# Performance work log

Measured on AMD Instinct MI355X. Metric: run time of the kernel, lower is better.

Reference implementation:

```python
import jax, jax.numpy as jnp
import numpy as np

B, S, DIM = 2, 2048, 2048
H, DH = 16, 128
FF = 4 * DIM
EPS = 1e-5


def layer_norm(x, w, b, eps=EPS):
    m = jnp.mean(x, axis=-1, keepdims=True)
    v = jnp.mean(jnp.square(x - m), axis=-1, keepdims=True)
    return (x - m) * jax.lax.rsqrt(v + eps) * w + b


def apply_rotary(x, cos, sin):
    # x: [B, H, S, DH]; cos/sin: [S, DH//2]; complex multiply on (even, odd) pairs
    x2 = x.reshape(*x.shape[:-1], DH // 2, 2)
    x0, x1 = x2[..., 0], x2[..., 1]
    c = cos[None, None, :, :]
    s = sin[None, None, :, :]
    r0 = x0 * c - x1 * s
    r1 = x0 * s + x1 * c
    return jnp.stack([r0, r1], axis=-1).reshape(x.shape)


def setup_inputs() -> dict:
    key = jax.random.key(0)
    ks = jax.random.split(key, 16)
    sc = 0.02
    pos = jnp.arange(S, dtype=jnp.float32)[:, None]
    inv_freq = 1.0 / (10000.0 ** (jnp.arange(0, DH // 2, dtype=jnp.float32) / (DH // 2)))
    ang = pos * inv_freq[None, :]
    return {
        "hidden_states": jax.random.normal(ks[0], (B, S, DIM), jnp.float32),
        "freqs_cos": jnp.cos(ang),
        "freqs_sin": jnp.sin(ang),
        "wq": jax.random.normal(ks[1], (DIM, H * DH), jnp.float32) * sc,
        "wk": jax.random.normal(ks[2], (DIM, H * DH), jnp.float32) * sc,
        "wv": jax.random.normal(ks[3], (DIM, H * DH), jnp.float32) * sc,
        "nq_w": jnp.ones((DH,), jnp.float32),
        "nq_b": jnp.zeros((DH,), jnp.float32),
        "nk_w": jnp.ones((DH,), jnp.float32),
        "nk_b": jnp.zeros((DH,), jnp.float32),
        "wo": jax.random.normal(ks[4], (H * DH, DIM), jnp.float32) * sc,
        "bo": jnp.zeros((DIM,), jnp.float32),
        "ln1_w": jnp.ones((DIM,), jnp.float32),
        "ln1_b": jnp.zeros((DIM,), jnp.float32),
        "ln3_w": jnp.ones((DIM,), jnp.float32),
        "ln3_b": jnp.zeros((DIM,), jnp.float32),
        "w1": jax.random.normal(ks[5], (DIM, FF), jnp.float32) * sc,
        "b1": jnp.zeros((FF,), jnp.float32),
        "w2": jax.random.normal(ks[6], (FF, DIM), jnp.float32) * sc,
        "b2": jnp.zeros((DIM,), jnp.float32),
    }


def reference(hidden_states, freqs_cos, freqs_sin, wq, wk, wv, nq_w, nq_b, nk_w, nk_b,
              wo, bo, ln1_w, ln1_b, ln3_w, ln3_b, w1, b1, w2, b2):
    x = hidden_states
    # --- self-attention branch ---
    n = layer_norm(x, ln1_w, ln1_b)                       # [B,S,DIM]
    q = (n @ wq).reshape(B, S, H, DH)
    k = (n @ wk).reshape(B, S, H, DH)
    v = (n @ wv).reshape(B, S, H, DH)
    # per-head QK LayerNorm (norm over dim_head)
    q = layer_norm(q, nq_w, nq_b)
    k = layer_norm(k, nk_w, nk_b)
    q = q.transpose(0, 2, 1, 3)                            # [B,H,S,DH]
    k = k.transpose(0, 2, 1, 3)
    v = v.transpose(0, 2, 1, 3)
    q = apply_rotary(q, freqs_cos, freqs_sin)
    k = apply_rotary(k, freqs_cos, freqs_sin)
    scale = DH ** -0.5
    scores = jnp.einsum("bhqd,bhkd->bhqk", q, k) * scale   # [B,H,S,S]
    probs = jax.nn.softmax(scores, axis=-1)
    attn = jnp.einsum("bhqk,bhkd->bhqd", probs, v)         # [B,H,S,DH]
    attn = attn.transpose(0, 2, 1, 3).reshape(B, S, H * DH)
    x = x + (attn @ wo + bo)
    # --- feed-forward branch ---
    n = layer_norm(x, ln3_w, ln3_b)
    h = jax.nn.gelu(n @ w1 + b1, approximate=False)
    x = x + (h @ w2 + b2)
    return x
```

## Files before the change

kernel.cpp:

```cpp
#include <hip/hip_runtime.h>
#include <hip/hip_bf16.h>
#include <stdint.h>

typedef __hip_bfloat16 bf16;
typedef float v4f __attribute__((ext_vector_type(4)));
typedef short v8s __attribute__((ext_vector_type(8)));

#define DEV __device__ __forceinline__

DEV float b2f(bf16 x) { return __bfloat162float(x); }
DEV bf16 f2b(float x) { return __float2bfloat16(x); }

DEV void load4(const float* p, float* f) {
  float4 t = *(const float4*)p;
  f[0] = t.x; f[1] = t.y; f[2] = t.z; f[3] = t.w;
}
DEV void load4(const bf16* p, float* f) {
  union { uint2 u; bf16 h[4]; } t;
  t.u = *(const uint2*)p;
#pragma unroll
  for (int i = 0; i < 4; i++) f[i] = b2f(t.h[i]);
}
DEV void load8(const float* p, float* f) {
  float4 a = ((const float4*)p)[0], b = ((const float4*)p)[1];
  f[0] = a.x; f[1] = a.y; f[2] = a.z; f[3] = a.w;
  f[4] = b.x; f[5] = b.y; f[6] = b.z; f[7] = b.w;
}
DEV void load8(const bf16* p, float* f) {
  union { uint4 u; bf16 h[8]; } t;
  t.u = *(const uint4*)p;
#pragma unroll
  for (int i = 0; i < 8; i++) f[i] = b2f(t.h[i]);
}
DEV void store4(bf16* p, const float* f) {
  union { uint2 u; bf16 h[4]; } t;
#pragma unroll
  for (int i = 0; i < 4; i++) t.h[i] = f2b(f[i]);
  *(uint2*)p = t.u;
}
DEV void store4(float* p, const float* f) {
  *(float4*)p = make_float4(f[0], f[1], f[2], f[3]);
}

DEV void gld_lds16(const bf16* g, bf16* l) {
  auto gp = reinterpret_cast<const __attribute__((address_space(1))) uint32_t*>(
      reinterpret_cast<uintptr_t>(g));
  auto lp = reinterpret_cast<__attribute__((address_space(3))) uint32_t*>(
      reinterpret_cast<uintptr_t>(l));
  __builtin_amdgcn_global_load_lds(gp, lp, 16, 0, 0);
}

template <typename XT>
__global__ __launch_bounds__(256)
void ln2048_kernel(const XT* __restrict__ x, const float* __restrict__ w,
                   const float* __restrict__ b, bf16* __restrict__ y) {
  const int N = 2048;
  int row = blockIdx.x, tid = threadIdx.x;
  const XT* xr = x + (size_t)row * N;
  bf16* yr = y + (size_t)row * N;
  float f[8], s = 0.f, ss = 0.f;
  load8(xr + tid * 8, f);
#pragma unroll
  for (int i = 0; i < 8; i++) { s += f[i]; ss += f[i] * f[i]; }
#pragma unroll
  for (int off = 32; off >= 1; off >>= 1) {
    s  += __shfl_xor(s, off, 64);
    ss += __shfl_xor(ss, off, 64);
  }
  __shared__ float red0[4], red1[4];
  int wv = tid >> 6;
  if ((tid & 63) == 0) { red0[wv] = s; red1[wv] = ss; }
  __syncthreads();
  s  = red0[0] + red0[1] + red0[2] + red0[3];
  ss = red1[0] + red1[1] + red1[2] + red1[3];
  float mean = s * (1.f / N);
  float var  = ss * (1.f / N) - mean * mean;
  float inv  = rsqrtf(var + 1e-5f);
  float wf[8], bf_[8];
  load8(w + tid * 8, wf);
  load8(b + tid * 8, bf_);
  union { uint4 u; bf16 h[8]; } vo;
#pragma unroll
  for (int i = 0; i < 8; i++)
    vo.h[i] = f2b((f[i] - mean) * inv * wf[i] + bf_[i]);
  ((uint4*)yr)[tid] = vo.u;
}

__global__ __launch_bounds__(256)
void headln_rope_kernel(bf16* __restrict__ q, const float* __restrict__ w,
                        const float* __restrict__ b, const float* __restrict__ fcos,
                        const float* __restrict__ fsin) {
  int tid = threadIdx.x;
  int wv = tid >> 6, ln = tid & 63;
  int idx = blockIdx.x * 4 + wv;
  int row = idx >> 4, h = idx & 15;
  int srow = row & 2047;
  bf16* p = q + (size_t)row * 2048 + h * 128 + ln * 2;
  union { unsigned int u; bf16 h2[2]; } v;
  v.u = *(const unsigned int*)p;
  float x0 = b2f(v.h2[0]), x1 = b2f(v.h2[1]);
  float s = x0 + x1, ss = x0 * x0 + x1 * x1;
#pragma unroll
  for (int off = 32; off >= 1; off >>= 1) {
    s  += __shfl_xor(s, off, 64);
    ss += __shfl_xor(ss, off, 64);
  }
  float mean = s * (1.f / 128.f);
  float var  = ss * (1.f / 128.f) - mean * mean;
  float inv  = rsqrtf(var + 1e-5f);
  float w0 = w[ln * 2], w1 = w[ln * 2 + 1];
  float b0 = b[ln * 2], b1 = b[ln * 2 + 1];
  x0 = (x0 - mean) * inv * w0 + b0;
  x1 = (x1 - mean) * inv * w1 + b1;
  float c  = fcos[srow * 64 + ln];
  float sn = fsin[srow * 64 + ln];
  v.h2[0] = f2b(x0 * c - x1 * sn);
  v.h2[1] = f2b(x0 * sn + x1 * c);
  *(unsigned int*)p = v.u;
}

__global__ __launch_bounds__(256)
void convT_kernel(const float* __restrict__ src, bf16* __restrict__ dst,
                  int K, int N) {
  __shared__ float T[64][65];
  int n0 = blockIdx.x * 64, k0 = blockIdx.y * 64;
  int t = threadIdx.x;
  int tr = t >> 4, tc4 = (t & 15) * 4;
#pragma unroll
  for (int it = 0; it < 4; it++) {
    float4 v = *(const float4*)&src[(size_t)(k0 + tr + 16 * it) * N + n0 + tc4];
    T[tr + 16 * it][tc4 + 0] = v.x;
    T[tr + 16 * it][tc4 + 1] = v.y;
    T[tr + 16 * it][tc4 + 2] = v.z;
    T[tr + 16 * it][tc4 + 3] = v.w;
  }
  __syncthreads();
#pragma unroll
  for (int it = 0; it < 4; it++) {
    int n = tr + 16 * it;
    union { uint2 u; bf16 h[4]; } o;
#pragma unroll
    for (int c = 0; c < 4; c++) o.h[c] = f2b(T[tc4 + c][n]);
    *(uint2*)&dst[(size_t)(n0 + n) * K + k0 + tc4] = o.u;
  }
}

template <int EPI, typename RT, typename OT>
__global__ __launch_bounds__(256, 2)
void mfma_gemm_kernel(const bf16* __restrict__ A, const bf16* __restrict__ BT,
                      OT* __restrict__ C, const float* __restrict__ bias,
                      const RT* __restrict__ res, int M, int N, int K) {
  __shared__ __align__(16) bf16 As[128 * 32];
  __shared__ __align__(16) bf16 Bs[128 * 32];
  int tid = threadIdx.x;
  int lane = tid & 63, wave = tid >> 6;
  int wr = wave >> 1, wc = wave & 1;
  int m0 = blockIdx.y * 128, n0 = blockIdx.x * 128;

  int ls_row = lane >> 2;
  int ls_k   = (lane & 3) * 8;
  int t0 = 2 * wave, t1 = 2 * wave + 1;
  const bf16* gA0 = A  + (size_t)(m0 + 16 * t0 + ls_row) * K + ls_k;
  const bf16* gA1 = A  + (size_t)(m0 + 16 * t1 + ls_row) * K + ls_k;
  const bf16* gB0 = BT + (size_t)(n0 + 16 * t0 + ls_row) * K + ls_k;
  const bf16* gB1 = BT + (size_t)(n0 + 16 * t1 + ls_row) * K + ls_k;
  bf16* lA0 = As + t0 * 512;
  bf16* lA1 = As + t1 * 512;
  bf16* lB0 = Bs + t0 * 512;
  bf16* lB1 = Bs + t1 * 512;

  int fr = lane & 15, fk = (lane >> 4) * 8;
  const bf16* pA = As + (wr * 64 + fr) * 32 + fk;
  const bf16* pB = Bs + (wc * 64 + fr) * 32 + fk;

  v4f acc[4][4];
#pragma unroll
  for (int i = 0; i < 4; i++)
#pragma unroll
    for (int j = 0; j < 4; j++) acc[i][j] = (v4f){0.f, 0.f, 0.f, 0.f};

  for (int k0 = 0; k0 < K; k0 += 32) {
    __syncthreads();
    gld_lds16(gA0, lA0); gld_lds16(gA1, lA1);
    gld_lds16(gB0, lB0); gld_lds16(gB1, lB1);
    gA0 += 32; gA1 += 32; gB0 += 32; gB1 += 32;
    __syncthreads();
    v8s af[4], bfr[4];
#pragma unroll
    for (int i = 0; i < 4; i++) af[i]  = *(const v8s*)(pA + i * 16 * 32);
#pragma unroll
    for (int j = 0; j < 4; j++) bfr[j] = *(const v8s*)(pB + j * 16 * 32);
#pragma unroll
    for (int i = 0; i < 4; i++)
#pragma unroll
      for (int j = 0; j < 4; j++)
        acc[i][j] = __builtin_amdgcn_mfma_f32_16x16x32_bf16(af[i], bfr[j],
                                                            acc[i][j], 0, 0, 0);
  }

  int rq = (lane >> 4) * 4;
#pragma unroll
  for (int j = 0; j < 4; j++) {
    int n = n0 + wc * 64 + j * 16 + (lane & 15);
    float bb = (EPI >= 1) ? bias[n] : 0.f;
#pragma unroll
    for (int i = 0; i < 4; i++) {
#pragma unroll
      for (int r = 0; r < 4; r++) {
        int m = m0 + wr * 64 + i * 16 + rq + r;
        float val = acc[i][j][r] + bb;
        if (EPI == 2)
          val = 0.5f * val * (1.f + erff(val * 0.70710678118654752f));
        if (EPI == 1) {
          if constexpr (__is_same(RT, float)) val += res[(size_t)m * N + n];
          else                                val += b2f(res[(size_t)m * N + n]);
        }
        if constexpr (__is_same(OT, float)) C[(size_t)m * N + n] = val;
        else                                C[(size_t)m * N + n] = f2b(val);
      }
    }
  }
}

template <int EPI, typename RT, typename OT>
__global__ __launch_bounds__(256)
void gemm_kernel(const bf16* __restrict__ A, const float* __restrict__ Bm,
                 OT* __restrict__ C, const float* __restrict__ bias,
                 const RT* __restrict__ res, int M, int N, int K) {
  const int BK = 32;
  __shared__ __align__(16) float As[BK][68];
  __shared__ __align__(16) float Bs[BK][68];
  int tid = threadIdx.x;
  int bm = blockIdx.y, bn = blockIdx.x;
  int tx = tid & 15, ty = tid >> 4;
  int am = tid >> 2, ak8 = (tid & 3) * 8;
  int bkr = tid >> 3, bn8 = (tid & 7) * 8;
  const bf16* Aptr = A + (size_t)(bm * 64 + am) * K + ak8;
  const float* Bptr = Bm + (size_t)bkr * N + bn * 64 + bn8;
  float acc[4][4] = {};
  for (int k0 = 0; k0 < K; k0 += BK) {
    float av[8], bv[8];
    load8(Aptr, av);
    load8(Bptr, bv);
    __syncthreads();
#pragma unroll
    for (int j = 0; j < 8; j++) As[ak8 + j][am] = av[j];
#pragma unroll
    for (int j = 0; j < 8; j++) Bs[bkr][bn8 + j] = bv[j];
    __syncthreads();
    Aptr += BK;
    Bptr += (size_t)BK * N;
#pragma unroll 8
    for (int kk = 0; kk < BK; kk++) {
      float a0[4], b0[4];
      *(float4*)a0 = *(const float4*)&As[kk][ty * 4];
      *(float4*)b0 = *(const float4*)&Bs[kk][tx * 4];
#pragma unroll
      for (int i = 0; i < 4; i++)
#pragma unroll
        for (int j = 0; j < 4; j++)
          acc[i][j] += a0[i] * b0[j];
    }
  }
  int m0 = bm * 64 + ty * 4, n0 = bn * 64 + tx * 4;
#pragma unroll
  for (int i = 0; i < 4; i++) {
    float r4[4];
#pragma unroll
    for (int j = 0; j < 4; j++) r4[j] = acc[i][j];
    if (EPI >= 1) {
      float bb[4];
      load4(bias + n0, bb);
#pragma unroll
      for (int j = 0; j < 4; j++) r4[j] += bb[j];
    }
    if (EPI == 2) {
#pragma unroll
      for (int j = 0; j < 4; j++)
        r4[j] = 0.5f * r4[j] * (1.f + erff(r4[j] * 0.70710678118654752f));
    }
    if (EPI == 1) {
      float rr[4];
      load4(res + (size_t)(m0 + i) * N + n0, rr);
#pragma unroll
      for (int j = 0; j < 4; j++) r4[j] += rr[j];
    }
    store4(&C[(size_t)(m0 + i) * N + n0], r4);
  }
}

__global__ __launch_bounds__(256, 2)
void attn_kernel(const bf16* __restrict__ q, const bf16* __restrict__ k,
                 const bf16* __restrict__ v, bf16* __restrict__ o) {
  const int S = 2048, HD = 2048;
  __shared__ __align__(16) char smem[49664];
  char* KsB = smem;
  char* VtB = smem + 16384;
  char* QPB = smem + 32768;
  float* Lp = (float*)(smem + 49152);

  int id = blockIdx.x;
  int swzb = (id & 7) * 128 + (id >> 3);
  int bh = swzb >> 5, qb = swzb & 31;
  int q0 = qb * 64;
  size_t base = (size_t)(bh >> 4) * S * HD + (size_t)(bh & 15) * 128;

  int tid = threadIdx.x;
  int lane = tid & 63, wave = tid >> 6;
  int wr = wave >> 1, wc = wave & 1;
  int fr = lane & 15, fg = lane >> 4;

  if (tid < 128) Lp[tid] = 0.f;

#pragma unroll
  for (int t = 0; t < 4; t++) {
    int ti = wave * 4 + t;
    int r = ti * 4 + fg;
    int cb = (fr * 16) ^ ((r & 7) << 4);
    gld_lds16(q + base + (size_t)(q0 + r) * HD + (cb >> 1),
              (bf16*)QPB + ti * 512);
  }
  __syncthreads();
  v8s qfrag[2][4];
#pragma unroll
  for (int i = 0; i < 2; i++)
#pragma unroll
    for (int kk = 0; kk < 4; kk++) {
      int row = wr * 32 + i * 16 + fr;
      int off = row * 256 + ((kk * 64 + fg * 16) ^ ((row & 7) << 4));
      qfrag[i][kk] = *(const v8s*)(QPB + off);
    }

  v4f oacc[2][4];
#pragma unroll
  for (int i = 0; i < 2; i++)
#pragma unroll
    for (int j = 0; j < 4; j++) oacc[i][j] = (v4f){0.f, 0.f, 0.f, 0.f};

  const float scale = 0.08838834764831845f;
  int vr0 = (tid & 15) * 4, vd0 = (tid >> 4) * 8;

  for (int kt = 0; kt < S; kt += 64) {
    __syncthreads();
#pragma unroll
    for (int t = 0; t < 4; t++) {
      int ti = wave * 4 + t;
      int r = ti * 4 + fg;
      int cb = (fr * 16) ^ ((r & 7) << 4);
      gld_lds16(k + base + (size_t)(kt + r) * HD + (cb >> 1),
                (bf16*)KsB + ti * 512);
    }
    union { uint4 u; bf16 h[8]; } vrow[4];
#pragma unroll
    for (int j = 0; j < 4; j++)
      vrow[j].u = *(const uint4*)&v[base + (size_t)(kt + vr0 + j) * HD + vd0];
#pragma unroll
    for (int c = 0; c < 8; c++) {
      int d = vd0 + c;
      union { uint2 u; bf16 h[4]; } pk;
#pragma unroll
      for (int j = 0; j < 4; j++) pk.h[j] = vrow[j].h[c];
      *(uint2*)(VtB + d * 128 + ((vr0 * 2) ^ ((d & 7) << 4))) = pk.u;
    }
    __syncthreads();

    v4f sacc[2][2];
#pragma unroll
    for (int i = 0; i < 2; i++)
#pragma unroll
      for (int j = 0; j < 2; j++) sacc[i][j] = (v4f){0.f, 0.f, 0.f, 0.f};
#pragma unroll
    for (int kk = 0; kk < 4; kk++) {
      v8s kf[2];
#pragma unroll
      for (int j = 0; j < 2; j++) {
        int row = wc * 32 + j * 16 + fr;
        int off = row * 256 + ((kk * 64 + fg * 16) ^ ((row & 7) << 4));
        kf[j] = *(const v8s*)(KsB + off);
      }
#pragma unroll
      for (int i = 0; i < 2; i++)
#pragma unroll
        for (int j = 0; j < 2; j++)
          sacc[i][j] = __builtin_amdgcn_mfma_f32_16x16x32_bf16(
              qfrag[i][kk], kf[j], sacc[i][j], 0, 0, 0);
    }

#pragma unroll
    for (int i = 0; i < 2; i++)
#pragma unroll
      for (int r = 0; r < 4; r++) {
        int qrow = wr * 32 + i * 16 + fg * 4 + r;
        float e0 = __expf(sacc[i][0][r] * scale);
        float e1 = __expf(sacc[i][1][r] * scale);
        int sw = (qrow & 7) << 4;
        int c0 = wc * 64 + fr * 2;
        *(bf16*)(QPB + qrow * 128 + (c0 ^ sw))        = f2b(e0);
        *(bf16*)(QPB + qrow * 128 + ((c0 + 32) ^ sw)) = f2b(e1);
        float s = e0 + e1;
        s += __shfl_xor(s, 1, 64);
        s += __shfl_xor(s, 2, 64);
        s += __shfl_xor(s, 4, 64);
        s += __shfl_xor(s, 8, 64);
        if (fr == 0) Lp[wc * 64 + qrow] += s;
      }
    __syncthreads();

#pragma unroll
    for (int kk2 = 0; kk2 < 2; kk2++) {
      v8s pf[2], vf[4];
#pragma unroll
      for (int i = 0; i < 2; i++) {
        int row = wr * 32 + i * 16 + fr;
        int off = row * 128 + ((kk2 * 64 + fg * 16) ^ ((row & 7) << 4));
        pf[i] = *(const v8s*)(QPB + off);
      }
#pragma unroll
      for (int j = 0; j < 4; j++) {
        int row = wc * 64 + j * 16 + fr;
        int off = row * 128 + ((kk2 * 64 + fg * 16) ^ ((row & 7) << 4));
        vf[j] = *(const v8s*)(VtB + off);
      }
#pragma unroll
      for (int i = 0; i < 2; i++)
#pragma unroll
        for (int j = 0; j < 4; j++)
          oacc[i][j] = __builtin_amdgcn_mfma_f32_16x16x32_bf16(
              pf[i], vf[j], oacc[i][j], 0, 0, 0);
    }
  }

#pragma unroll
  for (int i = 0; i < 2; i++)
#pragma unroll
    for (int r = 0; r < 4; r++) {
      int qrow = wr * 32 + i * 16 + fg * 4 + r;
      float linv = 1.f / (Lp[qrow] + Lp[64 + qrow]);
#pragma unroll
      for (int j = 0; j < 4; j++) {
        int d = wc * 64 + j * 16 + fr;
        o[base + (size_t)(q0 + qrow) * HD + d] = f2b(oacc[i][j][r] * linv);
      }
    }
}

extern "C" void kernel_launch(void* const* d_in, const int* in_sizes, int n_in,
                              void* d_out, int out_size, void* d_ws, size_t ws_size,
                              hipStream_t stream) {
  (void)in_sizes; (void)n_in; (void)out_size;
  const float* x    = (const float*)d_in[0];
  const float* fcos = (const float*)d_in[1];
  const float* fsin = (const float*)d_in[2];
  const float* wq   = (const float*)d_in[3];
  const float* wk   = (const float*)d_in[4];
  const float* wv   = (const float*)d_in[5];
  const float* nqw  = (const float*)d_in[6];
  const float* nqb  = (const float*)d_in[7];
  const float* nkw  = (const float*)d_in[8];
  const float* nkb  = (const float*)d_in[9];
  const float* wo   = (const float*)d_in[10];
  const float* bo   = (const float*)d_in[11];
  const float* ln1w = (const float*)d_in[12];
  const float* ln1b = (const float*)d_in[13];
  const float* ln3w = (const float*)d_in[14];
  const float* ln3b = (const float*)d_in[15];
  const float* w1   = (const float*)d_in[16];
  const float* b1   = (const float*)d_in[17];
  const float* w2   = (const float*)d_in[18];
  const float* b2   = (const float*)d_in[19];
  float* out = (float*)d_out;

  const size_t SEG = (size_t)4096 * 2048;
  bf16* base = (bf16*)d_ws;
  bf16* q        = base + 0 * SEG;
  bf16* k        = base + 1 * SEG;
  bf16* v        = base + 2 * SEG;
  bf16* n1       = base + 3 * SEG;
  bf16* attn_out = base + 3 * SEG;
  bf16* x2       = base + 4 * SEG;
  bf16* n3       = base + 5 * SEG;
  bf16* h        = base + 0 * SEG;

  dim3 blk(256);
  ln2048_kernel<float><<<4096, blk, 0, stream>>>(x, ln1w, ln1b, n1);

  bool mfma_path = ws_size >= (size_t)128 * 1024 * 1024;
  if (mfma_path) {
    bf16* W = base + 6 * SEG;
    bf16* wqT = W;
    bf16* wkT = W + 4 * 1024 * 1024;
    bf16* wvT = W + 8 * 1024 * 1024;
    bf16* woT = W;
    bf16* w1T = W;
    bf16* w2T = W;

    dim3 cg22(32, 32);
    dim3 g16(16, 32);
    dim3 g64(64, 32);

    convT_kernel<<<cg22, blk, 0, stream>>>(wq, wqT, 2048, 2048);
    convT_kernel<<<cg22, blk, 0, stream>>>(wk, wkT, 2048, 2048);
    convT_kernel<<<cg22, blk, 0, stream>>>(wv, wvT, 2048, 2048);
    mfma_gemm_kernel<0, float, bf16><<<g16, blk, 0, stream>>>(n1, wqT, q, nullptr, nullptr, 4096, 2048, 2048);
    mfma_gemm_kernel<0, float, bf16><<<g16, blk, 0, stream>>>(n1, wkT, k, nullptr, nullptr, 4096, 2048, 2048);
    mfma_gemm_kernel<0, float, bf16><<<g16, blk, 0, stream>>>(n1, wvT, v, nullptr, nullptr, 4096, 2048, 2048);
    headln_rope_kernel<<<16384, blk, 0, stream>>>(q, nqw, nqb, fcos, fsin);
    headln_rope_kernel<<<16384, blk, 0, stream>>>(k, nkw, nkb, fcos, fsin);
    attn_kernel<<<1024, blk, 0, stream>>>(q, k, v, attn_out);
    convT_kernel<<<cg22, blk, 0, stream>>>(wo, woT, 2048, 2048);
    mfma_gemm_kernel<1, float, bf16><<<g16, blk, 0, stream>>>(attn_out, woT, x2, bo, x, 4096, 2048, 2048);
    ln2048_kernel<bf16><<<4096, blk, 0, stream>>>(x2, ln3w, ln3b, n3);
    convT_kernel<<<dim3(128, 32), blk, 0, stream>>>(w1, w1T, 2048, 8192);
    mfma_gemm_kernel<2, float, bf16><<<g64, blk, 0, stream>>>(n3, w1T, h, b1, nullptr, 4096, 8192, 2048);
    convT_kernel<<<dim3(32, 128), blk, 0, stream>>>(w2, w2T, 8192, 2048);
    mfma_gemm_kernel<1, bf16, float><<<g16, blk, 0, stream>>>(h, w2T, out, b2, x2, 4096, 2048, 8192);
  } else {
    dim3 g2048(32, 64), g8192(128, 64);
    gemm_kernel<0, float, bf16><<<g2048, blk, 0, stream>>>(n1, wq, q, nullptr, nullptr, 4096, 2048, 2048);
    gemm_kernel<0, float, bf16><<<g2048, blk, 0, stream>>>(n1, wk, k, nullptr, nullptr, 4096, 2048, 2048);
    gemm_kernel<0, float, bf16><<<g2048, blk, 0, stream>>>(n1, wv, v, nullptr, nullptr, 4096, 2048, 2048);
    headln_rope_kernel<<<16384, blk, 0, stream>>>(q, nqw, nqb, fcos, fsin);
    headln_rope_kernel<<<16384, blk, 0, stream>>>(k, nkw, nkb, fcos, fsin);
    attn_kernel<<<1024, blk, 0, stream>>>(q, k, v, attn_out);
    gemm_kernel<1, float, bf16><<<g2048, blk, 0, stream>>>(attn_out, wo, x2, bo, x, 4096, 2048, 2048);
    ln2048_kernel<bf16><<<4096, blk, 0, stream>>>(x2, ln3w, ln3b, n3);
    gemm_kernel<2, float, bf16><<<g8192, blk, 0, stream>>>(n3, w1, h, b1, nullptr, 4096, 8192, 2048);
    gemm_kernel<1, bf16, float><<<g2048, blk, 0, stream>>>(h, w2, out, b2, x2, 4096, 2048, 8192);
  }
}
```

Baseline: 1.059 ms.

## Double-buffer K and register-prefetch V in attention kernel with priority hints

```diff
diff --git a/kernel.cpp b/kernel.cpp
--- a/kernel.cpp
+++ b/kernel.cpp
@@ -289,15 +289,18 @@
   }
 }
 
+#define VSWZ(r) (((((r) >> 3) ^ (r)) & 7) << 4)
+
 __global__ __launch_bounds__(256, 2)
 void attn_kernel(const bf16* __restrict__ q, const bf16* __restrict__ k,
                  const bf16* __restrict__ v, bf16* __restrict__ o) {
   const int S = 2048, HD = 2048;
-  __shared__ __align__(16) char smem[49664];
-  char* KsB = smem;
-  char* VtB = smem + 16384;
-  char* QPB = smem + 32768;
-  float* Lp = (float*)(smem + 49152);
+  __shared__ __align__(16) char smem[57856];
+  char* Ks0 = smem;
+  char* Ks1 = smem + 16384;
+  char* VtB = smem + 32768;
+  char* PB  = smem + 49152;
+  float* Lp = (float*)(smem + 57344);
 
   int id = blockIdx.x;
   int swzb = (id & 7) * 128 + (id >> 3);
@@ -312,15 +315,23 @@
 
   if (tid < 128) Lp[tid] = 0.f;
 
+  union V4U { uint4 u; bf16 h[8]; };
+  int vr0 = (tid & 15) * 4, vd0 = (tid >> 4) * 8;
+
 #pragma unroll
   for (int t = 0; t < 4; t++) {
     int ti = wave * 4 + t;
     int r = ti * 4 + fg;
     int cb = (fr * 16) ^ ((r & 7) << 4);
-    gld_lds16(q + base + (size_t)(q0 + r) * HD + (cb >> 1),
-              (bf16*)QPB + ti * 512);
-  }
+    gld_lds16(q + base + (size_t)(q0 + r) * HD + (cb >> 1), (bf16*)Ks0 + ti * 512);
+    gld_lds16(k + base + (size_t)r * HD + (cb >> 1), (bf16*)Ks1 + ti * 512);
+  }
+  V4U vA[4], vB[4];
+#pragma unroll
+  for (int j = 0; j < 4; j++)
+    vA[j].u = *(const uint4*)&v[base + (size_t)(vr0 + j) * HD + vd0];
   __syncthreads();
+
   v8s qfrag[2][4];
 #pragma unroll
   for (int i = 0; i < 2; i++)
@@ -328,8 +339,9 @@
     for (int kk = 0; kk < 4; kk++) {
       int row = wr * 32 + i * 16 + fr;
       int off = row * 256 + ((kk * 64 + fg * 16) ^ ((row & 7) << 4));
-      qfrag[i][kk] = *(const v8s*)(QPB + off);
-    }
+      qfrag[i][kk] = *(const v8s*)(Ks0 + off);
+    }
+  __syncthreads();
 
   v4f oacc[2][4];
 #pragma unroll
@@ -338,97 +350,106 @@
     for (int j = 0; j < 4; j++) oacc[i][j] = (v4f){0.f, 0.f, 0.f, 0.f};
 
   const float scale = 0.08838834764831845f;
-  int vr0 = (tid & 15) * 4, vd0 = (tid >> 4) * 8;
-
-  for (int kt = 0; kt < S; kt += 64) {
-    __syncthreads();
-#pragma unroll
-    for (int t = 0; t < 4; t++) {
-      int ti = wave * 4 + t;
-      int r = ti * 4 + fg;
-      int cb = (fr * 16) ^ ((r & 7) << 4);
-      gld_lds16(k + base + (size_t)(kt + r) * HD + (cb >> 1),
-                (bf16*)KsB + ti * 512);
-    }
-    union { uint4 u; bf16 h[8]; } vrow[4];
-#pragma unroll
-    for (int j = 0; j < 4; j++)
-      vrow[j].u = *(const uint4*)&v[base + (size_t)(kt + vr0 + j) * HD + vd0];
-#pragma unroll
-    for (int c = 0; c < 8; c++) {
-      int d = vd0 + c;
-      union { uint2 u; bf16 h[4]; } pk;
-#pragma unroll
-      for (int j = 0; j < 4; j++) pk.h[j] = vrow[j].h[c];
-      *(uint2*)(VtB + d * 128 + ((vr0 * 2) ^ ((d & 7) << 4))) = pk.u;
-    }
-    __syncthreads();
-
-    v4f sacc[2][2];
-#pragma unroll
-    for (int i = 0; i < 2; i++)
-#pragma unroll
-      for (int j = 0; j < 2; j++) sacc[i][j] = (v4f){0.f, 0.f, 0.f, 0.f};
-#pragma unroll
-    for (int kk = 0; kk < 4; kk++) {
-      v8s kf[2];
-#pragma unroll
-      for (int j = 0; j < 2; j++) {
-        int row = wc * 32 + j * 16 + fr;
-        int off = row * 256 + ((kk * 64 + fg * 16) ^ ((row & 7) << 4));
-        kf[j] = *(const v8s*)(KsB + off);
-      }
-#pragma unroll
-      for (int i = 0; i < 2; i++)
-#pragma unroll
-        for (int j = 0; j < 2; j++)
-          sacc[i][j] = __builtin_amdgcn_mfma_f32_16x16x32_bf16(
-              qfrag[i][kk], kf[j], sacc[i][j], 0, 0, 0);
-    }
-
-#pragma unroll
-    for (int i = 0; i < 2; i++)
-#pragma unroll
-      for (int r = 0; r < 4; r++) {
-        int qrow = wr * 32 + i * 16 + fg * 4 + r;
-        float e0 = __expf(sacc[i][0][r] * scale);
-        float e1 = __expf(sacc[i][1][r] * scale);
-        int sw = (qrow & 7) << 4;
-        int c0 = wc * 64 + fr * 2;
-        *(bf16*)(QPB + qrow * 128 + (c0 ^ sw))        = f2b(e0);
-        *(bf16*)(QPB + qrow * 128 + ((c0 + 32) ^ sw)) = f2b(e1);
-        float s = e0 + e1;
-        s += __shfl_xor(s, 1, 64);
-        s += __shfl_xor(s, 2, 64);
-        s += __shfl_xor(s, 4, 64);
-        s += __shfl_xor(s, 8, 64);
-        if (fr == 0) Lp[wc * 64 + qrow] += s;
-      }
-    __syncthreads();
-
-#pragma unroll
-    for (int kk2 = 0; kk2 < 2; kk2++) {
-      v8s pf[2], vf[4];
-#pragma unroll
-      for (int i = 0; i < 2; i++) {
-        int row = wr * 32 + i * 16 + fr;
-        int off = row * 128 + ((kk2 * 64 + fg * 16) ^ ((row & 7) << 4));
-        pf[i] = *(const v8s*)(QPB + off);
-      }
-#pragma unroll
-      for (int j = 0; j < 4; j++) {
-        int row = wc * 64 + j * 16 + fr;
-        int off = row * 128 + ((kk2 * 64 + fg * 16) ^ ((row & 7) << 4));
-        vf[j] = *(const v8s*)(VtB + off);
-      }
-#pragma unroll
-      for (int i = 0; i < 2; i++)
-#pragma unroll
-        for (int j = 0; j < 4; j++)
-          oacc[i][j] = __builtin_amdgcn_mfma_f32_16x16x32_bf16(
-              pf[i], vf[j], oacc[i][j], 0, 0, 0);
-    }
-  }
+
+#define ATTN_TILE(KT, KCUR, KNXT, VCUR, VNXT, STAGE_NEXT)                     \
+  {                                                                           \
+    _Pragma("unroll")                                                         \
+    for (int c = 0; c < 8; c++) {                                             \
+      int d = vd0 + c;                                                        \
+      union { uint2 u2; bf16 hh[4]; } pk;                                     \
+      _Pragma("unroll")                                                       \
+      for (int j = 0; j < 4; j++) pk.hh[j] = VCUR[j].h[c];                    \
+      *(uint2*)(VtB + d * 128 + ((vr0 * 2) ^ VSWZ(d))) = pk.u2;               \
+    }                                                                         \
+    if (STAGE_NEXT) {                                                         \
+      _Pragma("unroll")                                                       \
+      for (int t = 0; t < 4; t++) {                                           \
+        int ti = wave * 4 + t;                                                \
+        int r = ti * 4 + fg;                                                  \
+        int cb = (fr * 16) ^ ((r & 7) << 4);                                  \
+        gld_lds16(k + base + (size_t)((KT) + 64 + r) * HD + (cb >> 1),        \
+                  (bf16*)(KNXT) + ti * 512);                                  \
+      }                                                                       \
+      _Pragma("unroll")                                                       \
+      for (int j = 0; j < 4; j++)                                             \
+        VNXT[j].u =                                                           \
+            *(const uint4*)&v[base + (size_t)((KT) + 64 + vr0 + j) * HD + vd0]; \
+    }                                                                         \
+    v4f sacc[2][2];                                                           \
+    _Pragma("unroll")                                                         \
+    for (int i = 0; i < 2; i++)                                               \
+      _Pragma("unroll")                                                       \
+      for (int j = 0; j < 2; j++) sacc[i][j] = (v4f){0.f, 0.f, 0.f, 0.f};     \
+    __builtin_amdgcn_s_setprio(1);                                            \
+    _Pragma("unroll")                                                         \
+    for (int kk = 0; kk < 4; kk++) {                                          \
+      v8s kf[2];                                                              \
+      _Pragma("unroll")                                                       \
+      for (int j = 0; j < 2; j++) {                                           \
+        int row = wc * 32 + j * 16 + fr;                                      \
+        int off = row * 256 + ((kk * 64 + fg * 16) ^ ((row & 7) << 4));       \
+        kf[j] = *(const v8s*)((KCUR) + off);                                  \
+      }                                                                       \
+      _Pragma("unroll")                                                       \
+      for (int i = 0; i < 2; i++)                                             \
+        _Pragma("unroll")                                                     \
+        for (int j = 0; j < 2; j++)                                           \
+          sacc[i][j] = __builtin_amdgcn_mfma_f32_16x16x32_bf16(               \
+              qfrag[i][kk], kf[j], sacc[i][j], 0, 0, 0);                      \
+    }                                                                         \
+    __builtin_amdgcn_s_setprio(0);                                            \
+    _Pragma("unroll")                                                         \
+    for (int i = 0; i < 2; i++)                                               \
+      _Pragma("unroll")                                                       \
+      for (int r = 0; r < 4; r++) {                                           \
+        int qrow = wr * 32 + i * 16 + fg * 4 + r;                             \
+        float e0 = __expf(sacc[i][0][r] * scale);                             \
+        float e1 = __expf(sacc[i][1][r] * scale);                             \
+        int sw = VSWZ(qrow);                                                  \
+        int c0 = wc * 64 + fr * 2;                                            \
+        *(bf16*)(PB + qrow * 128 + (c0 ^ sw)) = f2b(e0);                      \
+        *(bf16*)(PB + qrow * 128 + ((c0 + 32) ^ sw)) = f2b(e1);               \
+        float s_ = e0 + e1;                                                   \
+        s_ += __shfl_xor(s_, 1, 64);                                          \
+        s_ += __shfl_xor(s_, 2, 64);                                          \
+        s_ += __shfl_xor(s_, 4, 64);                                          \
+        s_ += __shfl_xor(s_, 8, 64);                                          \
+        if (fr == 0) Lp[wc * 64 + qrow] += s_;                                \
+      }                                                                       \
+    __syncthreads();                                                          \
+    __builtin_amdgcn_s_setprio(1);                                            \
+    _Pragma("unroll")                                                         \
+    for (int kk2 = 0; kk2 < 2; kk2++) {                                       \
+      v8s pf[2], vf[4];                                                       \
+      _Pragma("unroll")                                                       \
+      for (int i = 0; i < 2; i++) {                                           \
+        int row = wr * 32 + i * 16 + fr;                                      \
+        int off = row * 128 + ((kk2 * 64 + fg * 16) ^ VSWZ(row));             \
+        pf[i] = *(const v8s*)(PB + off);                                      \
+      }                                                                       \
+      _Pragma("unroll")                                                       \
+      for (int j = 0; j < 4; j++) {                                           \
+        int row = wc * 64 + j * 16 + fr;                                      \
+        int off = row * 128 + ((kk2 * 64 + fg * 16) ^ VSWZ(row));             \
+        vf[j] = *(const v8s*)(VtB + off);                                     \
+      }                                                                       \
+      _Pragma("unroll")                                                       \
+      for (int i = 0; i < 2; i++)                                             \
+        _Pragma("unroll")                                                     \
+        for (int j = 0; j < 4; j++)                                           \
+          oacc[i][j] = __builtin_amdgcn_mfma_f32_16x16x32_bf16(               \
+              pf[i], vf[j], oacc[i][j], 0, 0, 0);                             \
+    }                                                                         \
+    __builtin_amdgcn_s_setprio(0);                                            \
+    __syncthreads();                                                          \
+  }
+
+  for (int tp = 0; tp < 16; tp++) {
+    int kt = tp * 128;
+    ATTN_TILE(kt, Ks1, Ks0, vA, vB, true);
+    ATTN_TILE(kt + 64, Ks0, Ks1, vB, vA, (tp < 15));
+  }
+#undef ATTN_TILE
 
 #pragma unroll
   for (int i = 0; i < 2; i++)
```

After: 1.026 ms. 1.03x faster.
